# Kernel tuning notes

Measured on AMD Instinct MI355X. Metric: run time of the kernel, lower is better.

The kernel has to match this reference:

```python
import jax, jax.numpy as jnp
import numpy as np

EMBED = 512  # scale uses embed_size**-0.5 per the original forward (NOT head_size)


def setup_inputs() -> dict:
    key = jax.random.key(0)
    k1, k2, k3, k4 = jax.random.split(key, 4)
    B, T, D, H = 8, 4096, EMBED, 64
    inputs = jax.random.normal(k1, (B, T, D), dtype=jnp.float32)
    Wq = jax.random.normal(k2, (D, H), dtype=jnp.float32) * (D ** -0.5)
    Wk = jax.random.normal(k3, (D, H), dtype=jnp.float32) * (D ** -0.5)
    Wv = jax.random.normal(k4, (D, H), dtype=jnp.float32) * (D ** -0.5)
    return {"inputs": inputs, "Wq": Wq, "Wk": Wk, "Wv": Wv}


def reference(inputs, Wq, Wk, Wv):
    # inputs: [B, T, D]; Wq/Wk/Wv: [D, H]
    B, T, D = inputs.shape
    q = inputs @ Wq  # [B, T, H]
    k = inputs @ Wk  # [B, T, H]
    v = inputs @ Wv  # [B, T, H]
    scale = jnp.asarray(D, inputs.dtype) ** -0.5  # original scales by embed_size**-0.5
    scores = jnp.einsum('bth,bsh->bts', q, k) * scale  # [B, T, T]
    causal = jnp.arange(T)[:, None] >= jnp.arange(T)[None, :]  # lower-triangular
    scores = jnp.where(causal, scores, jnp.asarray(-jnp.inf, scores.dtype))
    weights = jax.nn.softmax(scores, axis=-1)
    # dropout is identity in eval mode
    return weights @ v  # [B, T, H]
```

## Files before the change

kernel.cpp:

```cpp
#include <hip/hip_runtime.h>
#include <hip/hip_bf16.h>
#include <math.h>

#define TSEQ 4096
#define NB 8
#define DEM 512
#define HD 64
#define LP 72
#define WIP 136
#define WIMG 26624
#define QSZ ((size_t)NB * TSEQ * HD)

typedef __attribute__((ext_vector_type(8))) short short8;
typedef __attribute__((ext_vector_type(4))) short short4v;
typedef __attribute__((ext_vector_type(4))) float float4v;

__device__ __forceinline__ short f2bf(float f) {
    union { float f; unsigned u; } v; v.f = f;
    unsigned r = v.u + 0x7fffu + ((v.u >> 16) & 1u);
    return (short)(r >> 16);
}

__device__ __forceinline__ short8 pack8(float4 a, float4 b) {
    union { short8 s; __hip_bfloat162 h[4]; } u;
    u.h[0] = __float22bfloat162_rn(make_float2(a.x, a.y));
    u.h[1] = __float22bfloat162_rn(make_float2(a.z, a.w));
    u.h[2] = __float22bfloat162_rn(make_float2(b.x, b.y));
    u.h[3] = __float22bfloat162_rn(make_float2(b.z, b.w));
    return u.s;
}

__device__ __forceinline__ void gload_lds16(const void* g, void* l) {
    __builtin_amdgcn_global_load_lds(
        (const __attribute__((address_space(1))) unsigned int*)g,
        (__attribute__((address_space(3))) unsigned int*)l,
        16, 0, 0);
}

__device__ __host__ __forceinline__ int slot_base(int mq) {
    int grp = mq >> 3;
    return 4 * grp * (grp + 1) + (mq & 7) * (grp + 1);
}

__global__ __launch_bounds__(256) void wtr_kernel(
    const float* __restrict__ Wq, const float* __restrict__ Wk,
    const float* __restrict__ Wv, short* __restrict__ wimg)
{
    __shared__ float t[64][65];
    const int tid = threadIdx.x;
    const int kb = blockIdx.x;
    const int k0 = kb * 64;
    const int m = blockIdx.y;
    const int c = kb >> 1, half = kb & 1;
    const float* W = (m == 0) ? Wq : ((m == 1) ? Wk : Wv);
    const float sc = (m == 0) ? 0.044194173824159216f : 1.0f;

#pragma unroll
    for (int i = 0; i < 4; ++i) {
        int f = tid + 256 * i;
        int k = f >> 4, n4 = (f & 15) * 4;
        float4 wv = *(const float4*)&W[(k0 + k) * HD + n4];
        t[k][n4 + 0] = wv.x; t[k][n4 + 1] = wv.y;
        t[k][n4 + 2] = wv.z; t[k][n4 + 3] = wv.w;
    }
    __syncthreads();
#pragma unroll
    for (int i = 0; i < 4; ++i) {
        int f = tid + 256 * i;
        int n = f >> 4, k4 = (f & 15) * 4;
        short4v o;
        o[0] = f2bf(t[k4 + 0][n] * sc);
        o[1] = f2bf(t[k4 + 1][n] * sc);
        o[2] = f2bf(t[k4 + 2][n] * sc);
        o[3] = f2bf(t[k4 + 3][n] * sc);
        *(short4v*)&wimg[c * WIMG + (64 * m + n) * WIP + half * 64 + k4] = o;
    }
}

__global__ __launch_bounds__(256, 2) void qkv_mfma(
    const float* __restrict__ x, const short* __restrict__ wimg,
    short* __restrict__ q, short* __restrict__ k, short* __restrict__ vt)
{
    __shared__ alignas(16) short wlds[WIMG];

    const int tid = threadIdx.x;
    const int w = tid >> 6;
    const int l15 = tid & 15;
    const int quad = (tid >> 4) & 3;
    const int rbase = blockIdx.x * 64 + w * 16 + l15;

    const float* xr = x + (size_t)rbase * DEM;
    float4v acc[12] = {};

    for (int c = 0; c < 4; ++c) {
        __syncthreads();
        {
            const char* gsrc = (const char*)(wimg + c * WIMG) + tid * 16;
            char* ldst = (char*)wlds + tid * 16;
#pragma unroll
            for (int i = 0; i < 13; ++i)
                gload_lds16(gsrc + i * 4096, ldst + i * 4096);
        }
        __syncthreads();

#pragma unroll
        for (int ks = 0; ks < 4; ++ks) {
            const int k0 = c * 128 + ks * 32 + quad * 8;
            float4 xa = *(const float4*)&xr[k0];
            float4 xb = *(const float4*)&xr[k0 + 4];
            short8 xv = pack8(xa, xb);
            const int lk = ks * 32 + quad * 8;
#pragma unroll
            for (int mt = 0; mt < 12; ++mt) {
                short8 wf = *(const short8*)&wlds[(mt * 16 + l15) * WIP + lk];
                acc[mt] = __builtin_amdgcn_mfma_f32_16x16x32_bf16(wf, xv, acc[mt], 0, 0, 0);
            }
        }
    }

#pragma unroll
    for (int mt = 0; mt < 8; ++mt) {
        short* dst = (mt < 4) ? q : k;
        short4v o;
        o[0] = f2bf(acc[mt][0]); o[1] = f2bf(acc[mt][1]);
        o[2] = f2bf(acc[mt][2]); o[3] = f2bf(acc[mt][3]);
        *(short4v*)&dst[(size_t)rbase * HD + (mt & 3) * 16 + quad * 4] = o;
    }
    const int b = rbase >> 12, t = rbase & (TSEQ - 1);
#pragma unroll
    for (int mt = 8; mt < 12; ++mt) {
#pragma unroll
        for (int reg = 0; reg < 4; ++reg) {
            int d = (mt - 8) * 16 + quad * 4 + reg;
            vt[((size_t)(b * HD + d)) * TSEQ + t] = f2bf(acc[mt][reg]);
        }
    }
}

__global__ __launch_bounds__(256, 4) void flash_mfma(
    const short* __restrict__ qw, const short* __restrict__ kw,
    const short* __restrict__ vtw, float* __restrict__ out,
    float* __restrict__ pO, float* __restrict__ stS)
{
    __shared__ short kt[64 * LP];
    __shared__ short vt[64 * LP];
    __shared__ short pt[4][32 * LP];

    const int tid = threadIdx.x;
    const int w = tid >> 6;
    const int l15 = tid & 15;
    const int quad = (tid >> 4) & 3;
    const int bx = blockIdx.x;
    const int b = bx & 7;
    const int idx = bx >> 3;

    int mq, j;
    if (idx < 52) {
        int t = idx;
        mq = 31; j = 0;
#pragma unroll 1
        for (int mm = 31; mm >= 7; --mm) {
            int f = (2 * mm + 2) >> 4;
            if (t < f) { mq = mm; j = t; break; }
            t -= f;
        }
    } else {
        int t = idx - 52;
        int kc = t >> 2, p = t & 3;
        mq = 30 - kc - 8 * p;
        j = (2 * mq + 2) >> 4;
    }
    const int s0 = 16 * j;
    const int send = min(16 * (j + 1), 2 * mq + 2);
    const int r0 = mq * 128;
    const int slot = b * 80 + slot_base(mq) + j;

    short8 qf[2][2];
#pragma unroll
    for (int g = 0; g < 2; ++g) {
        const short* qrow = qw + ((size_t)(b * TSEQ + r0 + 32 * w + 16 * g + l15)) * HD;
        qf[g][0] = *(const short8*)(qrow + quad * 8);
        qf[g][1] = *(const short8*)(qrow + 32 + quad * 8);
    }

    float l_lane[2] = {0.f, 0.f};
    float4v O[2][4] = {};

    const int srow = tid >> 3, sc = tid & 7;
    const short* kbase = kw + (size_t)b * TSEQ * HD;
    const short* vbase = vtw + (size_t)b * HD * TSEQ;

    short8 kr0, kr1, vr0, vr1;
    {
        const short* kg = kbase + (size_t)(s0 * 64) * HD;
        const short* vg = vbase + s0 * 64;
        kr0 = *(const short8*)(kg + srow * HD + sc * 8);
        kr1 = *(const short8*)(kg + (srow + 32) * HD + sc * 8);
        vr0 = *(const short8*)(vg + (size_t)srow * TSEQ + sc * 8);
        vr1 = *(const short8*)(vg + (size_t)(srow + 32) * TSEQ + sc * 8);
    }

    for (int st = s0; st < send; ++st) {
        __syncthreads();
        *(short8*)&kt[srow * LP + sc * 8] = kr0;
        *(short8*)&kt[(srow + 32) * LP + sc * 8] = kr1;
        *(short8*)&vt[srow * LP + sc * 8] = vr0;
        *(short8*)&vt[(srow + 32) * LP + sc * 8] = vr1;
        __syncthreads();

        if (st + 1 < send) {
            const short* kg = kbase + (size_t)((st + 1) * 64) * HD;
            const short* vg = vbase + (st + 1) * 64;
            kr0 = *(const short8*)(kg + srow * HD + sc * 8);
            kr1 = *(const short8*)(kg + (srow + 32) * HD + sc * 8);
            vr0 = *(const short8*)(vg + (size_t)srow * TSEQ + sc * 8);
            vr1 = *(const short8*)(vg + (size_t)(srow + 32) * TSEQ + sc * 8);
        }

        float4v S[2][4] = {};
#pragma unroll
        for (int mt = 0; mt < 4; ++mt) {
            short8 a0 = *(const short8*)&kt[(mt * 16 + l15) * LP + quad * 8];
            short8 a1 = *(const short8*)&kt[(mt * 16 + l15) * LP + 32 + quad * 8];
            S[0][mt] = __builtin_amdgcn_mfma_f32_16x16x32_bf16(a0, qf[0][0], S[0][mt], 0, 0, 0);
            S[0][mt] = __builtin_amdgcn_mfma_f32_16x16x32_bf16(a1, qf[0][1], S[0][mt], 0, 0, 0);
            S[1][mt] = __builtin_amdgcn_mfma_f32_16x16x32_bf16(a0, qf[1][0], S[1][mt], 0, 0, 0);
            S[1][mt] = __builtin_amdgcn_mfma_f32_16x16x32_bf16(a1, qf[1][1], S[1][mt], 0, 0, 0);
        }

        if (st >= 2 * mq) {
            const int kb2 = st * 64;
#pragma unroll
            for (int g = 0; g < 2; ++g) {
                int qg = r0 + 32 * w + 16 * g + l15;
#pragma unroll
                for (int mt = 0; mt < 4; ++mt)
#pragma unroll
                    for (int r = 0; r < 4; ++r)
                        if (kb2 + mt * 16 + quad * 4 + r > qg) S[g][mt][r] = -INFINITY;
            }
        }

#pragma unroll
        for (int g = 0; g < 2; ++g) {
#pragma unroll
            for (int mt = 0; mt < 4; ++mt) {
                float p0 = __expf(S[g][mt][0]);
                float p1 = __expf(S[g][mt][1]);
                float p2 = __expf(S[g][mt][2]);
                float p3 = __expf(S[g][mt][3]);
                l_lane[g] += (p0 + p1) + (p2 + p3);
                short4v pk;
                pk[0] = f2bf(p0); pk[1] = f2bf(p1);
                pk[2] = f2bf(p2); pk[3] = f2bf(p3);
                *(short4v*)&pt[w][(16 * g + l15) * LP + mt * 16 + quad * 4] = pk;
            }
        }

#pragma unroll
        for (int kf = 0; kf < 2; ++kf) {
            short8 pa0 = *(const short8*)&pt[w][l15 * LP + kf * 32 + quad * 8];
            short8 pa1 = *(const short8*)&pt[w][(16 + l15) * LP + kf * 32 + quad * 8];
#pragma unroll
            for (int nt = 0; nt < 4; ++nt) {
                short8 vb = *(const short8*)&vt[(nt * 16 + l15) * LP + kf * 32 + quad * 8];
                O[0][nt] = __builtin_amdgcn_mfma_f32_16x16x32_bf16(pa0, vb, O[0][nt], 0, 0, 0);
                O[1][nt] = __builtin_amdgcn_mfma_f32_16x16x32_bf16(pa1, vb, O[1][nt], 0, 0, 0);
            }
        }
    }

    float lred[2];
#pragma unroll
    for (int g = 0; g < 2; ++g) {
        float rs = l_lane[g];
        rs += __shfl_xor(rs, 16, 64);
        rs += __shfl_xor(rs, 32, 64);
        lred[g] = rs;
    }

    if (mq <= 7) {
#pragma unroll
        for (int g = 0; g < 2; ++g) {
            float iv = 1.0f / lred[g];
#pragma unroll
            for (int r = 0; r < 4; ++r) {
                float ir = __shfl(iv, quad * 4 + r, 64);
                size_t row = (size_t)(b * TSEQ + r0 + 32 * w + 16 * g + quad * 4 + r) * HD;
#pragma unroll
                for (int nt = 0; nt < 4; ++nt)
                    out[row + nt * 16 + l15] = O[g][nt][r] * ir;
            }
        }
    } else {
        float* dest = pO + (size_t)slot * 128 * HD;
#pragma unroll
        for (int g = 0; g < 2; ++g) {
#pragma unroll
            for (int r = 0; r < 4; ++r) {
                size_t row = (size_t)(32 * w + 16 * g + quad * 4 + r) * HD;
#pragma unroll
                for (int nt = 0; nt < 4; ++nt)
                    dest[row + nt * 16 + l15] = O[g][nt][r];
            }
            if (quad == 0) stS[slot * 128 + 32 * w + 16 * g + l15] = lred[g];
        }
    }
}

__global__ __launch_bounds__(256) void merge_kernel(
    float* __restrict__ out, const float* __restrict__ pO,
    const float* __restrict__ stS)
{
    const int tid = threadIdx.x;
    const int bx = blockIdx.x;
    const int b = bx / 48, loc = bx - b * 48;
    const int t = 1024 + loc * 64 + (tid >> 2);
    const int dq = (tid & 3) * 16;
    const int mq = t >> 7, rr = t & 127;
    const int nseg = (2 * mq + 2 + 15) >> 4;
    const int sb = b * 80 + slot_base(mq);

    float denom = 0.f;
    for (int s = 0; s < nseg; ++s) denom += stS[(sb + s) * 128 + rr];
    float inv = 1.0f / denom;

    float4 o[4] = {};
    for (int s = 0; s < nseg; ++s) {
        const float4* pp = (const float4*)
            &pO[((size_t)(sb + s) * 128 + rr) * HD + dq];
#pragma unroll
        for (int i = 0; i < 4; ++i) {
            float4 p = pp[i];
            o[i].x += p.x; o[i].y += p.y;
            o[i].z += p.z; o[i].w += p.w;
        }
    }
    float4* op = (float4*)&out[((size_t)b * TSEQ + t) * HD + dq];
#pragma unroll
    for (int i = 0; i < 4; ++i) {
        o[i].x *= inv; o[i].y *= inv; o[i].z *= inv; o[i].w *= inv;
        op[i] = o[i];
    }
}

extern "C" void kernel_launch(void* const* d_in, const int* in_sizes, int n_in,
                              void* d_out, int out_size, void* d_ws, size_t ws_size,
                              hipStream_t stream) {
    const float* x  = (const float*)d_in[0];
    const float* Wq = (const float*)d_in[1];
    const float* Wk = (const float*)d_in[2];
    const float* Wv = (const float*)d_in[3];
    float* out = (float*)d_out;

    short* q  = (short*)d_ws;
    short* k  = q + QSZ;
    short* vt = k + QSZ;
    short* wimg = vt + QSZ;
    float* pO = (float*)(wimg + 4 * WIMG);
    float* stS = pO + (size_t)640 * 128 * HD;

    wtr_kernel<<<dim3(8, 3), 256, 0, stream>>>(Wq, Wk, Wv, wimg);
    qkv_mfma<<<dim3(NB * TSEQ / 64), 256, 0, stream>>>(x, wimg, q, k, vt);
    flash_mfma<<<dim3(640), 256, 0, stream>>>(q, k, vt, out, pO, stS);
    merge_kernel<<<dim3(384), 256, 0, stream>>>(out, pO, stS);
}
```

Before: 160.3 us.

## Split KV into 8-tile segments, use exp2 with folded log2e, MFMA row sums

```diff
diff --git a/kernel.cpp b/kernel.cpp
--- a/kernel.cpp
+++ b/kernel.cpp
@@ -10,6 +10,7 @@
 #define WIP 136
 #define WIMG 26624
 #define QSZ ((size_t)NB * TSEQ * HD)
+#define NSLOT 144
 
 typedef __attribute__((ext_vector_type(8))) short short8;
 typedef __attribute__((ext_vector_type(4))) short short4v;
@@ -30,6 +31,13 @@
     return u.s;
 }
 
+__device__ __forceinline__ short4v pack4(float a, float b, float c, float d) {
+    union { short4v s; __hip_bfloat162 h[2]; } u;
+    u.h[0] = __float22bfloat162_rn(make_float2(a, b));
+    u.h[1] = __float22bfloat162_rn(make_float2(c, d));
+    return u.s;
+}
+
 __device__ __forceinline__ void gload_lds16(const void* g, void* l) {
     __builtin_amdgcn_global_load_lds(
         (const __attribute__((address_space(1))) unsigned int*)g,
@@ -37,9 +45,9 @@
         16, 0, 0);
 }
 
-__device__ __host__ __forceinline__ int slot_base(int mq) {
-    int grp = mq >> 3;
-    return 4 * grp * (grp + 1) + (mq & 7) * (grp + 1);
+__device__ __host__ __forceinline__ int slot_base8(int mq) {
+    int a = mq >> 2, bq = mq & 3;
+    return (a + 1) * (2 * a + bq);
 }
 
 __global__ __launch_bounds__(256) void wtr_kernel(
@@ -53,7 +61,7 @@
     const int m = blockIdx.y;
     const int c = kb >> 1, half = kb & 1;
     const float* W = (m == 0) ? Wq : ((m == 1) ? Wk : Wv);
-    const float sc = (m == 0) ? 0.044194173824159216f : 1.0f;
+    const float sc = (m == 0) ? 0.063758715f : 1.0f;
 
 #pragma unroll
     for (int i = 0; i < 4; ++i) {
@@ -154,26 +162,20 @@
     const int b = bx & 7;
     const int idx = bx >> 3;
 
-    int mq, j;
-    if (idx < 52) {
+    int mq = 0, j = 0;
+    {
         int t = idx;
-        mq = 31; j = 0;
 #pragma unroll 1
-        for (int mm = 31; mm >= 7; --mm) {
-            int f = (2 * mm + 2) >> 4;
+        for (int mm = 31; mm >= 0; --mm) {
+            int f = (mm >> 2) + 1;
             if (t < f) { mq = mm; j = t; break; }
             t -= f;
         }
-    } else {
-        int t = idx - 52;
-        int kc = t >> 2, p = t & 3;
-        mq = 30 - kc - 8 * p;
-        j = (2 * mq + 2) >> 4;
-    }
-    const int s0 = 16 * j;
-    const int send = min(16 * (j + 1), 2 * mq + 2);
+    }
+    const int s0 = 8 * j;
+    const int send = min(8 * (j + 1), 2 * mq + 2);
     const int r0 = mq * 128;
-    const int slot = b * 80 + slot_base(mq) + j;
+    const int slot = b * NSLOT + slot_base8(mq) + j;
 
     short8 qf[2][2];
 #pragma unroll
@@ -183,8 +185,12 @@
         qf[g][1] = *(const short8*)(qrow + 32 + quad * 8);
     }
 
-    float l_lane[2] = {0.f, 0.f};
+    short8 ones;
+#pragma unroll
+    for (int i = 0; i < 8; ++i) ones[i] = (short)0x3F80;
+
     float4v O[2][4] = {};
+    float4v Lacc[2] = {};
 
     const int srow = tid >> 3, sc = tid & 7;
     const short* kbase = kw + (size_t)b * TSEQ * HD;
@@ -245,15 +251,12 @@
         for (int g = 0; g < 2; ++g) {
 #pragma unroll
             for (int mt = 0; mt < 4; ++mt) {
-                float p0 = __expf(S[g][mt][0]);
-                float p1 = __expf(S[g][mt][1]);
-                float p2 = __expf(S[g][mt][2]);
-                float p3 = __expf(S[g][mt][3]);
-                l_lane[g] += (p0 + p1) + (p2 + p3);
-                short4v pk;
-                pk[0] = f2bf(p0); pk[1] = f2bf(p1);
-                pk[2] = f2bf(p2); pk[3] = f2bf(p3);
-                *(short4v*)&pt[w][(16 * g + l15) * LP + mt * 16 + quad * 4] = pk;
+                float p0 = exp2f(S[g][mt][0]);
+                float p1 = exp2f(S[g][mt][1]);
+                float p2 = exp2f(S[g][mt][2]);
+                float p3 = exp2f(S[g][mt][3]);
+                *(short4v*)&pt[w][(16 * g + l15) * LP + mt * 16 + quad * 4] =
+                    pack4(p0, p1, p2, p3);
             }
         }
 
@@ -261,6 +264,8 @@
         for (int kf = 0; kf < 2; ++kf) {
             short8 pa0 = *(const short8*)&pt[w][l15 * LP + kf * 32 + quad * 8];
             short8 pa1 = *(const short8*)&pt[w][(16 + l15) * LP + kf * 32 + quad * 8];
+            Lacc[0] = __builtin_amdgcn_mfma_f32_16x16x32_bf16(pa0, ones, Lacc[0], 0, 0, 0);
+            Lacc[1] = __builtin_amdgcn_mfma_f32_16x16x32_bf16(pa1, ones, Lacc[1], 0, 0, 0);
 #pragma unroll
             for (int nt = 0; nt < 4; ++nt) {
                 short8 vb = *(const short8*)&vt[(nt * 16 + l15) * LP + kf * 32 + quad * 8];
@@ -270,28 +275,17 @@
         }
     }
 
-    float lred[2];
-#pragma unroll
-    for (int g = 0; g < 2; ++g) {
-        float rs = l_lane[g];
-        rs += __shfl_xor(rs, 16, 64);
-        rs += __shfl_xor(rs, 32, 64);
-        lred[g] = rs;
-    }
-
-    if (mq <= 7) {
-#pragma unroll
-        for (int g = 0; g < 2; ++g) {
-            float iv = 1.0f / lred[g];
+    if (mq <= 3) {
+#pragma unroll
+        for (int g = 0; g < 2; ++g)
 #pragma unroll
             for (int r = 0; r < 4; ++r) {
-                float ir = __shfl(iv, quad * 4 + r, 64);
+                float ir = 1.0f / Lacc[g][r];
                 size_t row = (size_t)(b * TSEQ + r0 + 32 * w + 16 * g + quad * 4 + r) * HD;
 #pragma unroll
                 for (int nt = 0; nt < 4; ++nt)
                     out[row + nt * 16 + l15] = O[g][nt][r] * ir;
             }
-        }
     } else {
         float* dest = pO + (size_t)slot * 128 * HD;
 #pragma unroll
@@ -302,8 +296,9 @@
 #pragma unroll
                 for (int nt = 0; nt < 4; ++nt)
                     dest[row + nt * 16 + l15] = O[g][nt][r];
-            }
-            if (quad == 0) stS[slot * 128 + 32 * w + 16 * g + l15] = lred[g];
+                if (l15 == quad * 4 + r)
+                    stS[slot * 128 + 32 * w + 16 * g + quad * 4 + r] = Lacc[g][r];
+            }
         }
     }
 }
@@ -314,12 +309,12 @@
 {
     const int tid = threadIdx.x;
     const int bx = blockIdx.x;
-    const int b = bx / 48, loc = bx - b * 48;
-    const int t = 1024 + loc * 64 + (tid >> 2);
+    const int b = bx / 56, loc = bx - b * 56;
+    const int t = 512 + loc * 64 + (tid >> 2);
     const int dq = (tid & 3) * 16;
     const int mq = t >> 7, rr = t & 127;
-    const int nseg = (2 * mq + 2 + 15) >> 4;
-    const int sb = b * 80 + slot_base(mq);
+    const int nseg = (mq >> 2) + 1;
+    const int sb = b * NSLOT + slot_base8(mq);
 
     float denom = 0.f;
     for (int s = 0; s < nseg; ++s) denom += stS[(sb + s) * 128 + rr];
@@ -358,10 +353,10 @@
     short* vt = k + QSZ;
     short* wimg = vt + QSZ;
     float* pO = (float*)(wimg + 4 * WIMG);
-    float* stS = pO + (size_t)640 * 128 * HD;
+    float* stS = pO + (size_t)NB * NSLOT * 128 * HD;
 
     wtr_kernel<<<dim3(8, 3), 256, 0, stream>>>(Wq, Wk, Wv, wimg);
     qkv_mfma<<<dim3(NB * TSEQ / 64), 256, 0, stream>>>(x, wimg, q, k, vt);
-    flash_mfma<<<dim3(640), 256, 0, stream>>>(q, k, vt, out, pO, stS);
-    merge_kernel<<<dim3(384), 256, 0, stream>>>(out, pO, stS);
-}
+    flash_mfma<<<dim3(NB * NSLOT), 256, 0, stream>>>(q, k, vt, out, pO, stS);
+    merge_kernel<<<dim3(448), 256, 0, stream>>>(out, pO, stS);
+}
```

Measured after the change: 201.1 us. 1.25x slower.
